# Kernel tuning notes

Measured on AMD Instinct MI355X. Metric: run time of the kernel, lower is better.

## Reference

```python
import jax, jax.numpy as jnp
import numpy as np

K = 128      # knowledge_n (= net1 = prednet output width)
LOW = 64     # low_dim
PP = 64      # pp_dim
STU = 50000  # student_n
EXER = 20000 # exer_n
S_RANGES = [(0, 9999), (10000, 19999)]
NR = len(S_RANGES)
B = 4096


def setup_inputs() -> dict:
    key = jax.random.key(0)
    ks = jax.random.split(key, 16)

    def xavier(k, shape):
        fan_in, fan_out = shape[-1], shape[-2] if len(shape) > 1 else shape[-1]
        lim = np.sqrt(6.0 / (fan_in + fan_out))
        return jax.random.uniform(k, shape, jnp.float32, -lim, lim)

    return {
        "stu_id": jax.random.randint(ks[0], (B,), 0, STU),
        "exer_id": jax.random.randint(ks[1], (B,), 0, EXER),
        "kn_emb": jnp.ones((B, K), jnp.float32),
        "student_emb": xavier(ks[2], (NR, STU, LOW)),          # ParameterList stacked
        "prompt_stu": xavier(ks[3], (STU, PP)),
        "knowledge_emb": jax.random.normal(ks[4], (K, LOW), jnp.float32),
        "k_difficulty": xavier(ks[5], (EXER, LOW)),
        "s_exer_vectors": jax.random.uniform(ks[6], (NR, PP), jnp.float32),
        "W1": xavier(ks[7], (K, K + LOW)),                      # prednet_full1 (no bias)
        "W2": xavier(ks[8], (K, K + LOW)),                      # prednet_full2 (no bias)
        "W3": xavier(ks[9], (1, K)),                            # prednet_full3
        "b3": jnp.zeros((1,), jnp.float32),
        "fc1_W": xavier(ks[10], (K, PP + K)),
        "fc1_b": jnp.zeros((K,), jnp.float32),
        "fc2_W": xavier(ks[11], (K, PP + K)),
        "fc2_b": jnp.zeros((K,), jnp.float32),
    }


def reference(stu_id, exer_id, kn_emb, student_emb, prompt_stu, knowledge_emb,
              k_difficulty, s_exer_vectors, W1, W2, W3, b3, fc1_W, fc1_b, fc2_W, fc2_b):
    sig = jax.nn.sigmoid
    kle = knowledge_emb  # [K, LOW]

    # --- student side ---
    # prompt_stu.repeat(NR, 1) then index_select == index prompt_stu with stu_id % STU
    p_stu = prompt_stu[stu_id % STU]                              # [B, PP]
    stu_cat = student_emb.reshape(NR * STU, LOW)                  # concat of ParameterList
    old_stu = sig(stu_cat[stu_id] @ kle.T)                        # [B, K]
    stu_e = sig(jnp.concatenate([p_stu, old_stu], 1) @ fc1_W.T + fc1_b)  # [B, K]

    # --- exercise side ---
    counts = np.array([r[1] - r[0] + 1 for r in S_RANGES])
    temp_vectors = jnp.repeat(s_exer_vectors, counts, axis=0, total_repeat_length=EXER)
    p_exer = sig(temp_vectors[exer_id])                           # [B, PP]
    old_exer = sig(sig(k_difficulty[exer_id]) @ kle.T)            # [B, K]
    exer_e = sig(jnp.concatenate([p_exer, old_exer], 1) @ fc2_W.T + fc2_b)  # [B, K]

    # --- per-concept interaction ---
    # cat([x_broadcast, kn_vector], 2) @ W.T splits into x @ Wa.T + kle @ Wb.T
    W1a, W1b = W1[:, :K], W1[:, K:]
    W2a, W2b = W2[:, :K], W2[:, K:]
    preference = sig((stu_e @ W1a.T)[:, None, :] + (kle @ W1b.T)[None, :, :])   # [B, K, K]
    diff = sig((exer_e @ W2a.T)[:, None, :] + (kle @ W2b.T)[None, :, :])        # [B, K, K]

    o = sig((preference - diff) @ W3.T + b3)                      # [B, K, 1]
    sum_out = jnp.sum(o * kn_emb[:, :, None], axis=1)             # [B, 1]
    count = jnp.sum(kn_emb, axis=1, keepdims=True)
    return sum_out / count
```

## Files before the change

kernel.cpp:

```cpp
#include <hip/hip_runtime.h>
#include <hip/hip_bf16.h>

#define STUN   50000
#define BATCH  4096
#define LOG2E  1.4426950408889634f

__device__ __forceinline__ float fexp2(float x){ return __builtin_amdgcn_exp2f(x); }
__device__ __forceinline__ float frcp (float x){ return __builtin_amdgcn_rcpf(x); }
__device__ __forceinline__ float fsig (float x){ return frcp(1.0f + fexp2(-LOG2E * x)); }

__global__ __launch_bounds__(128) void k_pre(
    const float* __restrict__ kle,
    const float* __restrict__ W1,
    const float* __restrict__ W2,
    const float* __restrict__ fc1_W,
    const float* __restrict__ fc2_W,
    float* __restrict__ kleT,
    float* __restrict__ fc1T,
    float* __restrict__ fc2T,
    float* __restrict__ W1aT,
    float* __restrict__ W2aT,
    float* __restrict__ E1i,
    float* __restrict__ E2i)
{
    const int bid = blockIdx.x;
    const int t   = threadIdx.x;
    if (bid < 64) {
        const int u = bid;
        kleT[u * 128 + t] = kle[t * 64 + u];
    } else if (bid < 256) {
        const int u = bid - 64;
        fc1T[u * 128 + t] = fc1_W[t * 192 + u];
    } else if (bid < 448) {
        const int u = bid - 256;
        fc2T[u * 128 + t] = fc2_W[t * 192 + u];
    } else if (bid < 576) {
        const int u = bid - 448;
        W1aT[u * 128 + t] = W1[t * 192 + u];
    } else if (bid < 704) {
        const int u = bid - 576;
        W2aT[u * 128 + t] = W2[t * 192 + u];
    } else if (bid < 832) {
        const int j = bid - 704;
        float acc = 0.f;
        #pragma unroll
        for (int u4 = 0; u4 < 16; ++u4) {
            const float4 kv = *(const float4*)&kle[t * 64 + u4 * 4];
            const float4 wv = *(const float4*)&W1[j * 192 + 128 + u4 * 4];
            acc += kv.x * wv.x + kv.y * wv.y + kv.z * wv.z + kv.w * wv.w;
        }
        E1i[((j >> 2) * 128 + t) * 4 + (j & 3)] = fexp2(-LOG2E * acc);
    } else {
        const int j = bid - 832;
        float acc = 0.f;
        #pragma unroll
        for (int u4 = 0; u4 < 16; ++u4) {
            const float4 kv = *(const float4*)&kle[t * 64 + u4 * 4];
            const float4 wv = *(const float4*)&W2[j * 192 + 128 + u4 * 4];
            acc += kv.x * wv.x + kv.y * wv.y + kv.z * wv.z + kv.w * wv.w;
        }
        E2i[((j >> 2) * 128 + t) * 4 + (j & 3)] = fexp2(-LOG2E * acc);
    }
}

__global__ __launch_bounds__(512, 4) void k_fused(
    const int*   __restrict__ stu_id,
    const int*   __restrict__ exer_id,
    const float* __restrict__ student_emb,
    const float* __restrict__ prompt_stu,
    const float* __restrict__ k_diff,
    const float* __restrict__ s_exer,
    const float* __restrict__ kleT,
    const float* __restrict__ fc1T,
    const float* __restrict__ fc2T,
    const float* __restrict__ W1aT,
    const float* __restrict__ W2aT,
    const float* __restrict__ fc1_b,
    const float* __restrict__ fc2_b,
    const float* __restrict__ E1i,
    const float* __restrict__ E2i,
    const float* __restrict__ W3,
    const float* __restrict__ b3,
    const float* __restrict__ kn,
    float* __restrict__ out)
{
    __shared__ __align__(16) float sh_in [4][64][8];
    __shared__ __align__(16) float sh_old[2][128][8];
    __shared__ __align__(16) float sh_e  [2][128][8];
    __shared__ __align__(16) float ses   [2][8][128];
    __shared__ float red_o[8][2];
    __shared__ float red_k[8][2];

    const int t  = threadIdx.x;
    const int b0 = blockIdx.x * 8;

    {
        const int g   = t >> 6;
        const int u   = t & 63;
        const int sid = stu_id[b0 + g];
        const int eid = exer_id[b0 + g];
        const int er  = (eid >= 10000) ? 1 : 0;
        sh_in[0][u][g] = student_emb[sid * 64 + u];
        sh_in[1][u][g] = fsig(k_diff[eid * 64 + u]);
        sh_in[2][u][g] = prompt_stu[(sid % STUN) * 64 + u];
        sh_in[3][u][g] = fsig(s_exer[er * 64 + u]);
    }
    __syncthreads();

    const int w    = t >> 6;
    const int half = w & 1;
    const int iqo  = w >> 1;
    const int l    = t & 63;
    const int ul   = l >> 4;
    const int bs   = (l >> 3) & 1;
    const int iql  = l & 7;
    const int iq   = iqo * 8 + iql;
    const int bq   = bs * 4;

    float a[4][4];

#define CLR { _Pragma("unroll") for (int c = 0; c < 4; ++c) \
              _Pragma("unroll") for (int b = 0; b < 4; ++b) a[c][b] = 0.f; }

#define FMAC(c, wc) { \
    a[c][0] = fmaf(wc, x0.x, a[c][0]); a[c][1] = fmaf(wc, x0.y, a[c][1]); \
    a[c][2] = fmaf(wc, x0.z, a[c][2]); a[c][3] = fmaf(wc, x0.w, a[c][3]); }

#define GSTEP(wp, xp) { \
    const float4 w4 = *(const float4*)(wp); \
    const float4 x0 = *(const float4*)(xp); \
    FMAC(0, w4.x); FMAC(1, w4.y); FMAC(2, w4.z); FMAC(3, w4.w); }

#define COMBINE { _Pragma("unroll") for (int c = 0; c < 4; ++c) \
    _Pragma("unroll") for (int b = 0; b < 4; ++b) { \
        float v = a[c][b]; \
        v += __shfl_xor(v, 16); \
        v += __shfl_xor(v, 32); \
        a[c][b] = v; } }

    CLR;
    #pragma unroll 4
    for (int u = ul; u < 64; u += 4)
        GSTEP(&kleT[u * 128 + iq * 4], &sh_in[half][u][bq]);
    COMBINE;
    if (ul == 0) {
        #pragma unroll
        for (int c = 0; c < 4; ++c)
            *(float4*)&sh_old[half][iq * 4 + c][bq] =
                make_float4(fsig(a[c][0]), fsig(a[c][1]), fsig(a[c][2]), fsig(a[c][3]));
    }
    __syncthreads();

    CLR;
    {
        const float* fcT = half ? fc2T : fc1T;
        #pragma unroll 4
        for (int u = ul; u < 64; u += 4)
            GSTEP(&fcT[u * 128 + iq * 4], &sh_in[2 + half][u][bq]);
        #pragma unroll 4
        for (int u = 64 + ul; u < 192; u += 4)
            GSTEP(&fcT[u * 128 + iq * 4], &sh_old[half][u - 64][bq]);
    }
    COMBINE;
    if (ul == 0) {
        const float* fcb = half ? fc2_b : fc1_b;
        #pragma unroll
        for (int c = 0; c < 4; ++c) {
            const float bias = fcb[iq * 4 + c];
            *(float4*)&sh_e[half][iq * 4 + c][bq] =
                make_float4(fsig(a[c][0] + bias), fsig(a[c][1] + bias),
                            fsig(a[c][2] + bias), fsig(a[c][3] + bias));
        }
    }
    __syncthreads();

    CLR;
    {
        const float* WT = half ? W2aT : W1aT;
        #pragma unroll 4
        for (int u = ul; u < 128; u += 4)
            GSTEP(&WT[u * 128 + iq * 4], &sh_e[half][u][bq]);
    }
    COMBINE;
    if (ul == 0) {
        #pragma unroll
        for (int c = 0; c < 4; ++c) {
            #pragma unroll
            for (int b = 0; b < 4; ++b)
                ses[half][bq + b][iq * 4 + c] = fexp2(-LOG2E * a[c][b]);
        }
    }
#undef CLR
#undef FMAC
#undef GSTEP
#undef COMBINE
    __syncthreads();

    const int k  = t & 127;
    const int bh = t >> 7;
    const int i0 = bh * 2;

    const float4* E1v = (const float4*)E1i + k;
    const float4* E2v = (const float4*)E2i + k;
    const float* s1a = &ses[0][i0 + 0][0];
    const float* s2a = &ses[1][i0 + 0][0];
    const float* s1b = &ses[0][i0 + 1][0];
    const float* s2b = &ses[1][i0 + 1][0];

    float acc0 = 0.f, acc1 = 0.f;

#define COMP(acc, s1c, s2c, e1c, e2c, w3c) { \
        const float uu = (s1c) * (e1c); \
        const float vv = (s2c) * (e2c); \
        const float dd = frcp((1.f + uu) * (1.f + vv)); \
        acc = fmaf((vv - uu) * dd, (w3c), acc); }

    #pragma unroll 4
    for (int j4 = 0; j4 < 32; ++j4) {
        const int j = j4 * 4;
        const float4 e1 = E1v[j4 * 128];
        const float4 e2 = E2v[j4 * 128];
        const float4 w3 = *(const float4*)&W3[j];
        const float4 p1a = *(const float4*)&s1a[j];
        const float4 p2a = *(const float4*)&s2a[j];
        const float4 p1b = *(const float4*)&s1b[j];
        const float4 p2b = *(const float4*)&s2b[j];
        COMP(acc0, p1a.x, p2a.x, e1.x, e2.x, w3.x);
        COMP(acc0, p1a.y, p2a.y, e1.y, e2.y, w3.y);
        COMP(acc0, p1a.z, p2a.z, e1.z, e2.z, w3.z);
        COMP(acc0, p1a.w, p2a.w, e1.w, e2.w, w3.w);
        COMP(acc1, p1b.x, p2b.x, e1.x, e2.x, w3.x);
        COMP(acc1, p1b.y, p2b.y, e1.y, e2.y, w3.y);
        COMP(acc1, p1b.z, p2b.z, e1.z, e2.z, w3.z);
        COMP(acc1, p1b.w, p2b.w, e1.w, e2.w, w3.w);
    }
#undef COMP

    const float bb3 = b3[0];
    const float o0  = fsig(acc0 + bb3);
    const float o1  = fsig(acc1 + bb3);
    const float kn0 = kn[(b0 + i0 + 0) * 128 + k];
    const float kn1 = kn[(b0 + i0 + 1) * 128 + k];
    float co0 = o0 * kn0, ck0 = kn0;
    float co1 = o1 * kn1, ck1 = kn1;
    #pragma unroll
    for (int off = 1; off < 64; off <<= 1) {
        co0 += __shfl_xor(co0, off);
        ck0 += __shfl_xor(ck0, off);
        co1 += __shfl_xor(co1, off);
        ck1 += __shfl_xor(ck1, off);
    }
    if ((t & 63) == 0) {
        red_o[w][0] = co0; red_o[w][1] = co1;
        red_k[w][0] = ck0; red_k[w][1] = ck1;
    }
    __syncthreads();
    if (t < 8) {
        const int p = t >> 1;
        const int i = t & 1;
        const float so = red_o[p * 2][i] + red_o[p * 2 + 1][i];
        const float sk = red_k[p * 2][i] + red_k[p * 2 + 1][i];
        out[b0 + t] = so / sk;
    }
}

extern "C" void kernel_launch(void* const* d_in, const int* in_sizes, int n_in,
                              void* d_out, int out_size, void* d_ws, size_t ws_size,
                              hipStream_t stream)
{
    const int*   stu_id      = (const int*)  d_in[0];
    const int*   exer_id     = (const int*)  d_in[1];
    const float* kn_emb      = (const float*)d_in[2];
    const float* student_emb = (const float*)d_in[3];
    const float* prompt_stu  = (const float*)d_in[4];
    const float* kle         = (const float*)d_in[5];
    const float* k_diff      = (const float*)d_in[6];
    const float* s_exer      = (const float*)d_in[7];
    const float* W1          = (const float*)d_in[8];
    const float* W2          = (const float*)d_in[9];
    const float* W3          = (const float*)d_in[10];
    const float* b3          = (const float*)d_in[11];
    const float* fc1_W       = (const float*)d_in[12];
    const float* fc1_b       = (const float*)d_in[13];
    const float* fc2_W       = (const float*)d_in[14];
    const float* fc2_b       = (const float*)d_in[15];
    float* out = (float*)d_out;

    float* ws   = (float*)d_ws;
    float* kleT = ws;
    float* fc1T = kleT + 8192;
    float* fc2T = fc1T + 24576;
    float* W1aT = fc2T + 24576;
    float* W2aT = W1aT + 16384;
    float* E1i  = W2aT + 16384;
    float* E2i  = E1i  + 16384;

    k_pre  <<<960, 128, 0, stream>>>(kle, W1, W2, fc1_W, fc2_W,
                                     kleT, fc1T, fc2T, W1aT, W2aT, E1i, E2i);
    k_fused<<<BATCH / 8, 512, 0, stream>>>(stu_id, exer_id, student_emb, prompt_stu,
                                           k_diff, s_exer, kleT, fc1T, fc2T,
                                           W1aT, W2aT, fc1_b, fc2_b,
                                           E1i, E2i, W3, b3, kn_emb, out);
}
```

Measured before the change: 49.14 us.

## Split interaction j-loop across thread quarters and reuse E loads over eight batch rows

The final per-concept loop is restructured so each thread covers a quarter of the j range for all 8 batch rows, instead of the full j range for 2 rows. Each E1/E2 float4 global load is then reused across 8 rows rather than 2, cutting global/L2 traffic. Partial sums are combined through a new shared-memory reduction buffer before the sigmoid and weighted sum. The shared arrays sh_old and sh_e are also padded from 8 to 12, likely to avoid bank conflicts. The cost is more shared memory, an extra barrier and 8 accumulators per thread, which raises register pressure.

```diff
diff --git a/kernel.cpp b/kernel.cpp
--- a/kernel.cpp
+++ b/kernel.cpp
@@ -85,11 +85,12 @@
     float* __restrict__ out)
 {
     __shared__ __align__(16) float sh_in [4][64][8];
-    __shared__ __align__(16) float sh_old[2][128][8];
-    __shared__ __align__(16) float sh_e  [2][128][8];
+    __shared__ __align__(16) float sh_old[2][128][12];
+    __shared__ __align__(16) float sh_e  [2][128][12];
     __shared__ __align__(16) float ses   [2][8][128];
-    __shared__ float red_o[8][2];
-    __shared__ float red_k[8][2];
+    __shared__ __align__(16) float red   [4][8][128];
+    __shared__ float red2_o[8][2];
+    __shared__ float red2_k[8][2];
 
     const int t  = threadIdx.x;
     const int b0 = blockIdx.x * 8;
@@ -197,69 +198,79 @@
     __syncthreads();
 
     const int k  = t & 127;
-    const int bh = t >> 7;
-    const int i0 = bh * 2;
+    const int jq = t >> 7;
 
     const float4* E1v = (const float4*)E1i + k;
     const float4* E2v = (const float4*)E2i + k;
-    const float* s1a = &ses[0][i0 + 0][0];
-    const float* s2a = &ses[1][i0 + 0][0];
-    const float* s1b = &ses[0][i0 + 1][0];
-    const float* s2b = &ses[1][i0 + 1][0];
-
-    float acc0 = 0.f, acc1 = 0.f;
-
-#define COMP(acc, s1c, s2c, e1c, e2c, w3c) { \
+
+    float acc[8];
+    #pragma unroll
+    for (int b = 0; b < 8; ++b) acc[b] = 0.f;
+
+#define COMP(acc_, s1c, s2c, e1c, e2c, w3c) { \
         const float uu = (s1c) * (e1c); \
         const float vv = (s2c) * (e2c); \
         const float dd = frcp((1.f + uu) * (1.f + vv)); \
-        acc = fmaf((vv - uu) * dd, (w3c), acc); }
-
-    #pragma unroll 4
-    for (int j4 = 0; j4 < 32; ++j4) {
-        const int j = j4 * 4;
+        acc_ = fmaf((vv - uu) * dd, (w3c), acc_); }
+
+    #pragma unroll 2
+    for (int i = 0; i < 8; ++i) {
+        const int j4 = jq * 8 + i;
+        const int j  = j4 * 4;
         const float4 e1 = E1v[j4 * 128];
         const float4 e2 = E2v[j4 * 128];
         const float4 w3 = *(const float4*)&W3[j];
-        const float4 p1a = *(const float4*)&s1a[j];
-        const float4 p2a = *(const float4*)&s2a[j];
-        const float4 p1b = *(const float4*)&s1b[j];
-        const float4 p2b = *(const float4*)&s2b[j];
-        COMP(acc0, p1a.x, p2a.x, e1.x, e2.x, w3.x);
-        COMP(acc0, p1a.y, p2a.y, e1.y, e2.y, w3.y);
-        COMP(acc0, p1a.z, p2a.z, e1.z, e2.z, w3.z);
-        COMP(acc0, p1a.w, p2a.w, e1.w, e2.w, w3.w);
-        COMP(acc1, p1b.x, p2b.x, e1.x, e2.x, w3.x);
-        COMP(acc1, p1b.y, p2b.y, e1.y, e2.y, w3.y);
-        COMP(acc1, p1b.z, p2b.z, e1.z, e2.z, w3.z);
-        COMP(acc1, p1b.w, p2b.w, e1.w, e2.w, w3.w);
+        #pragma unroll
+        for (int b = 0; b < 8; ++b) {
+            const float4 p1 = *(const float4*)&ses[0][b][j];
+            const float4 p2 = *(const float4*)&ses[1][b][j];
+            COMP(acc[b], p1.x, p2.x, e1.x, e2.x, w3.x);
+            COMP(acc[b], p1.y, p2.y, e1.y, e2.y, w3.y);
+            COMP(acc[b], p1.z, p2.z, e1.z, e2.z, w3.z);
+            COMP(acc[b], p1.w, p2.w, e1.w, e2.w, w3.w);
+        }
     }
 #undef COMP
 
-    const float bb3 = b3[0];
-    const float o0  = fsig(acc0 + bb3);
-    const float o1  = fsig(acc1 + bb3);
-    const float kn0 = kn[(b0 + i0 + 0) * 128 + k];
-    const float kn1 = kn[(b0 + i0 + 1) * 128 + k];
-    float co0 = o0 * kn0, ck0 = kn0;
-    float co1 = o1 * kn1, ck1 = kn1;
     #pragma unroll
-    for (int off = 1; off < 64; off <<= 1) {
-        co0 += __shfl_xor(co0, off);
-        ck0 += __shfl_xor(ck0, off);
-        co1 += __shfl_xor(co1, off);
-        ck1 += __shfl_xor(ck1, off);
-    }
-    if ((t & 63) == 0) {
-        red_o[w][0] = co0; red_o[w][1] = co1;
-        red_k[w][0] = ck0; red_k[w][1] = ck1;
+    for (int b = 0; b < 8; ++b) red[jq][b][k] = acc[b];
+    __syncthreads();
+
+    {
+        const float bb3 = b3[0];
+        float co[2], ck[2];
+        #pragma unroll
+        for (int h = 0; h < 2; ++h) {
+            const int item = t + h * 512;
+            const int b    = item >> 7;
+            const int kk   = item & 127;
+            const float s  = red[0][b][kk] + red[1][b][kk]
+                           + red[2][b][kk] + red[3][b][kk];
+            const float o  = fsig(s + bb3);
+            const float kv = kn[(b0 + b) * 128 + kk];
+            co[h] = o * kv;
+            ck[h] = kv;
+        }
+        #pragma unroll
+        for (int off = 1; off < 64; off <<= 1) {
+            co[0] += __shfl_xor(co[0], off);
+            ck[0] += __shfl_xor(ck[0], off);
+            co[1] += __shfl_xor(co[1], off);
+            ck[1] += __shfl_xor(ck[1], off);
+        }
+        if ((t & 63) == 0) {
+            const int b_  = w >> 1;
+            const int kh  = w & 1;
+            red2_o[b_][kh]     = co[0];
+            red2_k[b_][kh]     = ck[0];
+            red2_o[b_ + 4][kh] = co[1];
+            red2_k[b_ + 4][kh] = ck[1];
+        }
     }
     __syncthreads();
     if (t < 8) {
-        const int p = t >> 1;
-        const int i = t & 1;
-        const float so = red_o[p * 2][i] + red_o[p * 2 + 1][i];
-        const float sk = red_k[p * 2][i] + red_k[p * 2 + 1][i];
+        const float so = red2_o[t][0] + red2_o[t][1];
+        const float sk = red2_k[t][0] + red2_k[t][1];
         out[b0 + t] = so / sk;
     }
 }
```

Result: faster. 47.42 us (-3.5%).
